# Kernel optimization log

Measured on AMD Instinct MI355X. Metric: run time of the kernel, lower is better.

Reference implementation:

```python
import jax, jax.numpy as jnp
import numpy as np

NEG_INF = -1e9


def setup_inputs() -> dict:
    key = jax.random.key(0)
    ks = jax.random.split(key, 12)
    B, S, D, H = 32, 2048, 512, 512
    enc_outs = jax.random.normal(ks[0], (B, S, D), dtype=jnp.float32)
    num_sent = jnp.maximum(jax.random.randint(ks[1], (B,), 0, S), 1).astype(jnp.int64)
    s = 1.0 / np.sqrt(H)
    return {
        "enc_outs": enc_outs,
        "num_sent": num_sent,
        "num_pred": 8,
        "init_h": jax.random.normal(ks[2], (1, H), dtype=jnp.float32) * s,
        "init_c": jax.random.normal(ks[3], (1, H), dtype=jnp.float32) * s,
        "init_in": jax.random.normal(ks[4], (D,), dtype=jnp.float32) * s,
        "W_ih": jax.random.uniform(ks[5], (4 * H, D), jnp.float32, -s, s),
        "W_hh": jax.random.uniform(ks[6], (4 * H, H), jnp.float32, -s, s),
        "b_ih": jax.random.uniform(ks[7], (4 * H,), jnp.float32, -s, s),
        "b_hh": jax.random.uniform(ks[8], (4 * H,), jnp.float32, -s, s),
        "attn_Wq": jax.random.uniform(ks[9], (H, D), jnp.float32, -s, s),
        "score_W": jax.random.uniform(ks[10], (1, H), jnp.float32, -s, s),
        "score_b": jax.random.uniform(ks[11], (1,), jnp.float32, -s, s),
    }


def reference(enc_outs, num_sent, num_pred, init_h, init_c, init_in,
              W_ih, W_hh, b_ih, b_hh, attn_Wq, score_W, score_b):
    B, S, D = enc_outs.shape
    H = init_h.shape[1]
    # rep_mask: True where sentence index is valid
    mask = jnp.arange(S)[None, :] < num_sent[:, None]  # [B, S]

    def lstm_cell(x, h, c):
        gates = x @ W_ih.T + b_ih + h @ W_hh.T + b_hh  # [B, 4H]
        i, f, g, o = jnp.split(gates, 4, axis=-1)
        i, f, o = jax.nn.sigmoid(i), jax.nn.sigmoid(f), jax.nn.sigmoid(o)
        c_new = f * c + i * jnp.tanh(g)
        return o * jnp.tanh(c_new), c_new

    h0 = jnp.broadcast_to(init_h[0], (B, H))
    c0 = jnp.broadcast_to(init_c[0], (B, H))
    in0 = jnp.broadcast_to(init_in, (B, D))

    def step(carry, _):
        h, c, lstm_in = carry
        h, c = lstm_cell(lstm_in, h, c)
        # glimpse attention: bilinear score, masked softmax over sentences
        q = h @ attn_Wq  # [B, D]
        logits = jnp.einsum('bd,bsd->bs', q, enc_outs)
        logits = jnp.where(mask, logits, NEG_INF)
        attn = jax.nn.softmax(logits, axis=-1)
        out = jnp.einsum('bs,bsd->bd', attn, enc_outs)  # [B, D]
        score = out @ score_W.T + score_b  # [B, 1]
        return (h, c, out), score

    _, scores = jax.lax.scan(step, (h0, c0, in0), None, length=int(num_pred))
    return scores  # [num_pred, B, 1]
```

## Files before the change

kernel.cpp:

```cpp
#include <hip/hip_runtime.h>
#include <math.h>

#define B    32
#define S    2048
#define D    512
#define H    512
#define NP   8
#define NSL  32
#define HSL  16
#define NBT  4
#define BG   8
#define NCH  8
#define SCHUNK 256

__device__ __forceinline__ float sigmoidf_(float x) {
  return 1.0f / (1.0f + __expf(-x));
}

__global__ __launch_bounds__(256)
void k_init(const float* __restrict__ W_ih, const float* __restrict__ W_hh,
            const float* __restrict__ init_h, const float* __restrict__ init_c,
            const float* __restrict__ init_in, const int* __restrict__ ns_raw,
            float* __restrict__ Wt, float* __restrict__ hbuf, float* __restrict__ cbuf,
            float* __restrict__ xin0, int* __restrict__ ns) {
  __shared__ float tbuf[64][65];
  const int blk = blockIdx.x, tid = threadIdx.x;
  const int jt = blk & 31, kt = blk >> 5;
  const int j0 = jt * 64, k0 = kt * 64;
  const int r0 = tid >> 6, cc = tid & 63;
  for (int rr = r0; rr < 64; rr += 4) {
    int j = j0 + rr, k = k0 + cc;
    tbuf[rr][cc] = (k < 512) ? W_ih[(size_t)j * 512 + k]
                             : W_hh[(size_t)j * 512 + (k - 512)];
  }
  __syncthreads();
  for (int rr = r0; rr < 64; rr += 4)
    Wt[(size_t)(k0 + rr) * 2048 + j0 + cc] = tbuf[cc][rr];

  int idx = blk * 256 + tid;
  if (idx < B * H) {
    int d = idx & 511;
    hbuf[idx] = init_h[d];
    cbuf[idx] = init_c[d];
    xin0[idx] = init_in[d];
  }
  if (idx == 0) {
    bool is64 = (ns_raw[1] == 0);
    for (int i = 0; i < B; ++i) ns[i] = is64 ? ns_raw[2 * i] : ns_raw[i];
  }
}

__global__ __launch_bounds__(512, 1)
void k_step(const float* __restrict__ xin0, const float* __restrict__ bih,
            const float* __restrict__ bhh, const float* __restrict__ Wq,
            const float* __restrict__ scW, const float* __restrict__ scb,
            const float* __restrict__ Wt,
            const float* __restrict__ ch_m, const float* __restrict__ ch_l,
            const float* __restrict__ ch_o,
            float* __restrict__ hbuf, float* __restrict__ cbuf,
            float* __restrict__ qpart, float* __restrict__ out, int t) {
  __shared__ float X[BG][1024];
  __shared__ float gacc[8][64][9];
  __shared__ float gl[4][16][8];
  __shared__ float hl[8][16];
  __shared__ float sred[8][8];

  const int tid = threadIdx.x;
  const int sl = blockIdx.x >> 2;
  const int bg = blockIdx.x & 3;
  const int b0 = bg * BG;

  if (t == 0) {
    #pragma unroll
    for (int bl = 0; bl < BG; ++bl)
      X[bl][tid] = xin0[(b0 + bl) * 512 + tid];
  } else {
    const float swd = scW[tid];
    #pragma unroll
    for (int bl = 0; bl < BG; ++bl) {
      const int b = b0 + bl;
      float M = -1e30f;
      #pragma unroll
      for (int c = 0; c < NCH; ++c) M = fmaxf(M, ch_m[b * NCH + c]);
      float e[NCH]; float L = 0.f;
      #pragma unroll
      for (int c = 0; c < NCH; ++c) {
        e[c] = __expf(ch_m[b * NCH + c] - M);
        L += ch_l[b * NCH + c] * e[c];
      }
      float v = 0.f;
      #pragma unroll
      for (int c = 0; c < NCH; ++c)
        v += ch_o[((size_t)(b * NCH + c)) * 512 + tid] * e[c];
      v *= (1.0f / L);
      X[bl][tid] = v;
      float p = v * swd;
      #pragma unroll
      for (int off = 32; off > 0; off >>= 1) p += __shfl_xor(p, off);
      if ((tid & 63) == 0) sred[tid >> 6][bl] = p;
    }
  }
  if (t < NP) {
    const float4* hsrc = (const float4*)(hbuf + (t & 1) * (B * 512));
    #pragma unroll
    for (int it = 0; it < 2; ++it) {
      int idx = it * 512 + tid;
      int bl = idx >> 7;
      int off = idx & 127;
      float4 hv = hsrc[(b0 + bl) * 128 + off];
      *(float4*)&X[bl][512 + off * 4] = hv;
    }
  }
  __syncthreads();

  if (t >= 1 && tid < BG) {
    float s = 0.f;
    #pragma unroll
    for (int w = 0; w < 8; ++w) s += sred[w][tid];
    if (sl == 0) out[(t - 1) * B + b0 + tid] = s + scb[0];
  }
  if (t >= NP) return;

  {
    const int jloc = tid & 63;
    const int kc = tid >> 6;
    const int gi = jloc >> 4, ho = jloc & 15;
    const int jg = gi * 512 + sl * HSL + ho;
    const int k0c = kc * 128;
    const float* wp = Wt + (size_t)k0c * 2048 + jg;
    float acc[BG] = {0, 0, 0, 0, 0, 0, 0, 0};
    for (int kk = 0; kk < 32; ++kk) {
      float wv0 = wp[(size_t)(kk * 4 + 0) * 2048];
      float wv1 = wp[(size_t)(kk * 4 + 1) * 2048];
      float wv2 = wp[(size_t)(kk * 4 + 2) * 2048];
      float wv3 = wp[(size_t)(kk * 4 + 3) * 2048];
      #pragma unroll
      for (int bl = 0; bl < BG; ++bl) {
        const float4 xv = *(const float4*)&X[bl][k0c + kk * 4];
        acc[bl] += wv0 * xv.x + wv1 * xv.y + wv2 * xv.z + wv3 * xv.w;
      }
    }
    #pragma unroll
    for (int bl = 0; bl < BG; ++bl) gacc[kc][jloc][bl] = acc[bl];
  }
  __syncthreads();

  {
    const int bl = tid >> 6, jloc = tid & 63;
    const int gi = jloc >> 4, ho = jloc & 15;
    const int jg = gi * 512 + sl * HSL + ho;
    float g = bih[jg] + bhh[jg];
    #pragma unroll
    for (int kc = 0; kc < 8; ++kc) g += gacc[kc][jloc][bl];
    gl[gi][ho][bl] = g;
  }
  __syncthreads();

  if (tid < 128) {
    const int ho = tid & 15, bl = tid >> 4;
    const int bglob = b0 + bl, hid = sl * HSL + ho;
    float i_ = sigmoidf_(gl[0][ho][bl]);
    float f_ = sigmoidf_(gl[1][ho][bl]);
    float g_ = tanhf(gl[2][ho][bl]);
    float o_ = sigmoidf_(gl[3][ho][bl]);
    float cv = cbuf[bglob * 512 + hid];
    float cn = f_ * cv + i_ * g_;
    cbuf[bglob * 512 + hid] = cn;
    float hv = o_ * tanhf(cn);
    hbuf[((t + 1) & 1) * (B * 512) + bglob * 512 + hid] = hv;
    hl[bl][ho] = hv;
  }
  __syncthreads();

  {
    float w[HSL];
    #pragma unroll
    for (int ho = 0; ho < HSL; ++ho)
      w[ho] = Wq[(size_t)(sl * HSL + ho) * 512 + tid];
    #pragma unroll
    for (int bl = 0; bl < BG; ++bl) {
      float acc = 0.f;
      #pragma unroll
      for (int ho = 0; ho < HSL; ++ho) acc += hl[bl][ho] * w[ho];
      qpart[((size_t)sl * B + b0 + bl) * 512 + tid] = acc;
    }
  }
}

__global__ __launch_bounds__(512, 1)
void k_attn(const float* __restrict__ enc, const float* __restrict__ qpart,
            const int* __restrict__ ns_buf, float* __restrict__ ch_m,
            float* __restrict__ ch_l, float* __restrict__ ch_o) {
  __shared__ float q_lds[512];
  __shared__ float wm[8], wl[8];
  __shared__ float wo[8][512];
  const int b  = blockIdx.x >> 3;
  const int ch = blockIdx.x & 7;
  const int tid = threadIdx.x;
  const int lane = tid & 63;
  const int wv = tid >> 6;

  {
    float s = 0.f;
    #pragma unroll
    for (int sl = 0; sl < NSL; ++sl)
      s += qpart[((size_t)sl * B + b) * 512 + tid];
    q_lds[tid] = s;
  }
  __syncthreads();

  const float4 qa  = *(const float4*)&q_lds[lane * 8];
  const float4 qb4 = *(const float4*)&q_lds[lane * 8 + 4];

  const int s0 = ch * SCHUNK;
  const int nsb = ns_buf[b];
  float m = -1e30f, l = 0.f;
  float o0=0,o1=0,o2=0,o3=0,o4=0,o5=0,o6=0,o7=0;

  const int send = min(s0 + SCHUNK, nsb);
  const size_t rowbase = (size_t)b * S;

  int r = s0 + 2 * wv;
  if (r < send) {
    bool has1 = (r + 1 < send);
    const float4* p0 = (const float4*)(enc + (rowbase + r) * 512 + lane * 8);
    const float4* p1 = (const float4*)(enc + (rowbase + (has1 ? r + 1 : r)) * 512 + lane * 8);
    float4 a0 = p0[0], a1 = p0[1];
    float4 c0 = p1[0], c1 = p1[1];
    while (true) {
      const int rn = r + 16;
      const bool hasn = (rn < send);
      float4 na0, na1, nc0, nc1;
      bool nhas1 = false;
      if (hasn) {
        nhas1 = (rn + 1 < send);
        const float4* f0 = (const float4*)(enc + (rowbase + rn) * 512 + lane * 8);
        const float4* f1 = (const float4*)(enc + (rowbase + (nhas1 ? rn + 1 : rn)) * 512 + lane * 8);
        na0 = f0[0]; na1 = f0[1]; nc0 = f1[0]; nc1 = f1[1];
      }
      float d0 = qa.x*a0.x + qa.y*a0.y + qa.z*a0.z + qa.w*a0.w
               + qb4.x*a1.x + qb4.y*a1.y + qb4.z*a1.z + qb4.w*a1.w;
      float d1 = qa.x*c0.x + qa.y*c0.y + qa.z*c0.z + qa.w*c0.w
               + qb4.x*c1.x + qb4.y*c1.y + qb4.z*c1.z + qb4.w*c1.w;
      #pragma unroll
      for (int off = 32; off > 0; off >>= 1) {
        d0 += __shfl_xor(d0, off);
        d1 += __shfl_xor(d1, off);
      }
      if (!has1) d1 = -1e30f;
      float nm = fmaxf(m, fmaxf(d0, d1));
      float sc = __expf(m - nm);
      float w0 = __expf(d0 - nm);
      float w1 = __expf(d1 - nm);
      l = l * sc + w0 + w1;
      o0 = o0*sc + w0*a0.x + w1*c0.x; o1 = o1*sc + w0*a0.y + w1*c0.y;
      o2 = o2*sc + w0*a0.z + w1*c0.z; o3 = o3*sc + w0*a0.w + w1*c0.w;
      o4 = o4*sc + w0*a1.x + w1*c1.x; o5 = o5*sc + w0*a1.y + w1*c1.y;
      o6 = o6*sc + w0*a1.z + w1*c1.z; o7 = o7*sc + w0*a1.w + w1*c1.w;
      m = nm;
      if (!hasn) break;
      r = rn; has1 = nhas1;
      a0 = na0; a1 = na1; c0 = nc0; c1 = nc1;
    }
  }
  if (lane == 0) { wm[wv] = m; wl[wv] = l; }
  float4* wop = (float4*)&wo[wv][lane * 8];
  wop[0] = make_float4(o0, o1, o2, o3);
  wop[1] = make_float4(o4, o5, o6, o7);
  __syncthreads();

  float M = wm[0];
  #pragma unroll
  for (int w = 1; w < 8; ++w) M = fmaxf(M, wm[w]);
  float e[8]; float L = 0.f;
  #pragma unroll
  for (int w = 0; w < 8; ++w) { e[w] = __expf(wm[w] - M); L += wl[w] * e[w]; }
  if (tid == 0) { ch_m[b * NCH + ch] = M; ch_l[b * NCH + ch] = L; }
  float v = 0.f;
  #pragma unroll
  for (int w = 0; w < 8; ++w) v += wo[w][tid] * e[w];
  ch_o[((size_t)(b * NCH + ch)) * 512 + tid] = v;
}

extern "C" void kernel_launch(void* const* d_in, const int* in_sizes, int n_in,
                              void* d_out, int out_size, void* d_ws, size_t ws_size,
                              hipStream_t stream) {
  const float* enc     = (const float*)d_in[0];
  const int*   ns_raw  = (const int*)d_in[1];
  const float* init_h  = (const float*)d_in[3];
  const float* init_c  = (const float*)d_in[4];
  const float* init_in = (const float*)d_in[5];
  const float* W_ih    = (const float*)d_in[6];
  const float* W_hh    = (const float*)d_in[7];
  const float* b_ih    = (const float*)d_in[8];
  const float* b_hh    = (const float*)d_in[9];
  const float* Wq      = (const float*)d_in[10];
  const float* score_W = (const float*)d_in[11];
  const float* score_b = (const float*)d_in[12];
  float* out = (float*)d_out;

  float* ws    = (float*)d_ws;
  float* Wt    = ws;
  float* hbuf  = ws + 2097152;
  float* cbuf  = ws + 2129920;
  float* xin0  = ws + 2146304;
  float* qpart = ws + 2162688;
  float* ch_m  = ws + 2686976;
  float* ch_l  = ws + 2687232;
  float* ch_o  = ws + 2687488;
  int*   ns    = (int*)(ws + 2818560);

  k_init<<<512, 256, 0, stream>>>(W_ih, W_hh, init_h, init_c, init_in, ns_raw,
                                  Wt, hbuf, cbuf, xin0, ns);
  for (int t = 0; t < NP; ++t) {
    k_step<<<NSL * NBT, 512, 0, stream>>>(xin0, b_ih, b_hh, Wq, score_W, score_b, Wt,
                                          ch_m, ch_l, ch_o, hbuf, cbuf, qpart, out, t);
    k_attn<<<B * NCH, 512, 0, stream>>>(enc, qpart, ns, ch_m, ch_l, ch_o);
  }
  k_step<<<NSL * NBT, 512, 0, stream>>>(xin0, b_ih, b_hh, Wq, score_W, score_b, Wt,
                                        ch_m, ch_l, ch_o, hbuf, cbuf, qpart, out, NP);
}
```

Baseline: 354.1 us.

## Fuse per-step LSTM and attention kernels into one persistent kernel with grid barriers

Replaces the 17 alternating k_step/k_attn launches with a single persistent 256-block kernel that loops over the 8 prediction steps. Stages are separated by a software grid barrier built from agent-scope atomic counters. The cell state and the Wq slice stay in registers across steps, and the batch group per block is halved so 256 blocks cover both phases. This removes per-launch overhead and the final extra step kernel. In exchange it depends on all 256 blocks being co-resident, and it adds atomic polling cost plus relaxed-atomic loads and stores for data passed between blocks.

```diff
diff --git a/kernel.cpp b/kernel.cpp
--- a/kernel.cpp
+++ b/kernel.cpp
@@ -3,26 +3,48 @@
 
 #define B    32
 #define S    2048
-#define D    512
-#define H    512
 #define NP   8
 #define NSL  32
 #define HSL  16
-#define NBT  4
-#define BG   8
+#define BG   4
 #define NCH  8
 #define SCHUNK 256
+#define NBLK 256
+#define NTHR 512
+#define NBAR 16
+
+#define AT_LD(p)   __hip_atomic_load((p), __ATOMIC_RELAXED, __HIP_MEMORY_SCOPE_AGENT)
+#define AT_ST(p,v) __hip_atomic_store((p), (v), __ATOMIC_RELAXED, __HIP_MEMORY_SCOPE_AGENT)
 
 __device__ __forceinline__ float sigmoidf_(float x) {
   return 1.0f / (1.0f + __expf(-x));
 }
 
+__device__ __forceinline__ void gbar(int* cnt, int bi) {
+  asm volatile("s_waitcnt vmcnt(0) lgkmcnt(0)" ::: "memory");
+  __syncthreads();
+  if (threadIdx.x == 0) {
+    int* base = cnt + bi * 128;
+    __hip_atomic_fetch_add(base + (blockIdx.x & 7) * 16, 1,
+                           __ATOMIC_RELAXED, __HIP_MEMORY_SCOPE_AGENT);
+    int s;
+    do {
+      s = 0;
+      #pragma unroll
+      for (int q = 0; q < 8; ++q) s += AT_LD(base + q * 16);
+      if (s < NBLK) __builtin_amdgcn_s_sleep(2);
+    } while (s < NBLK);
+  }
+  __syncthreads();
+  asm volatile("" ::: "memory");
+}
+
 __global__ __launch_bounds__(256)
 void k_init(const float* __restrict__ W_ih, const float* __restrict__ W_hh,
-            const float* __restrict__ init_h, const float* __restrict__ init_c,
-            const float* __restrict__ init_in, const int* __restrict__ ns_raw,
-            float* __restrict__ Wt, float* __restrict__ hbuf, float* __restrict__ cbuf,
-            float* __restrict__ xin0, int* __restrict__ ns) {
+            const float* __restrict__ init_h, const float* __restrict__ init_in,
+            const int* __restrict__ ns_raw,
+            float* __restrict__ Wt, float* __restrict__ hbuf,
+            float* __restrict__ xin0, int* __restrict__ ns, int* __restrict__ cnt) {
   __shared__ float tbuf[64][65];
   const int blk = blockIdx.x, tid = threadIdx.x;
   const int jt = blk & 31, kt = blk >> 5;
@@ -38,248 +60,279 @@
     Wt[(size_t)(k0 + rr) * 2048 + j0 + cc] = tbuf[cc][rr];
 
   int idx = blk * 256 + tid;
-  if (idx < B * H) {
+  if (idx < B * 512) {
     int d = idx & 511;
     hbuf[idx] = init_h[d];
-    cbuf[idx] = init_c[d];
     xin0[idx] = init_in[d];
   }
+  if (idx < NBAR * 128) cnt[idx] = 0;
   if (idx == 0) {
     bool is64 = (ns_raw[1] == 0);
     for (int i = 0; i < B; ++i) ns[i] = is64 ? ns_raw[2 * i] : ns_raw[i];
   }
 }
 
-__global__ __launch_bounds__(512, 1)
-void k_step(const float* __restrict__ xin0, const float* __restrict__ bih,
-            const float* __restrict__ bhh, const float* __restrict__ Wq,
-            const float* __restrict__ scW, const float* __restrict__ scb,
-            const float* __restrict__ Wt,
-            const float* __restrict__ ch_m, const float* __restrict__ ch_l,
-            const float* __restrict__ ch_o,
-            float* __restrict__ hbuf, float* __restrict__ cbuf,
-            float* __restrict__ qpart, float* __restrict__ out, int t) {
+__global__ __launch_bounds__(NTHR, 1)
+void k_persist(const float* __restrict__ enc, const float* __restrict__ init_c,
+               const float* __restrict__ bih, const float* __restrict__ bhh,
+               const float* __restrict__ Wq, const float* __restrict__ scW,
+               const float* __restrict__ scb, const float* __restrict__ Wt,
+               const float* __restrict__ xin0,
+               float* __restrict__ out, float* __restrict__ hbuf,
+               float* __restrict__ qpart, float* __restrict__ ch_m,
+               float* __restrict__ ch_l, float* __restrict__ ch_o,
+               const int* __restrict__ ns, int* __restrict__ cnt) {
   __shared__ float X[BG][1024];
-  __shared__ float gacc[8][64][9];
-  __shared__ float gl[4][16][8];
-  __shared__ float hl[8][16];
-  __shared__ float sred[8][8];
+  __shared__ float gacc[8][64][5];
+  __shared__ float gl[4][HSL][BG];
+  __shared__ float hl[BG][HSL];
+  __shared__ float sred[8][BG];
+  __shared__ float q_lds[512];
+  __shared__ float wm[8], wl[8];
+  __shared__ float wo[8][512];
 
   const int tid = threadIdx.x;
-  const int sl = blockIdx.x >> 2;
-  const int bg = blockIdx.x & 3;
-  const int b0 = bg * BG;
-
-  if (t == 0) {
-    #pragma unroll
-    for (int bl = 0; bl < BG; ++bl)
-      X[bl][tid] = xin0[(b0 + bl) * 512 + tid];
-  } else {
-    const float swd = scW[tid];
-    #pragma unroll
-    for (int bl = 0; bl < BG; ++bl) {
-      const int b = b0 + bl;
-      float M = -1e30f;
-      #pragma unroll
-      for (int c = 0; c < NCH; ++c) M = fmaxf(M, ch_m[b * NCH + c]);
-      float e[NCH]; float L = 0.f;
-      #pragma unroll
-      for (int c = 0; c < NCH; ++c) {
-        e[c] = __expf(ch_m[b * NCH + c] - M);
-        L += ch_l[b * NCH + c] * e[c];
-      }
-      float v = 0.f;
-      #pragma unroll
-      for (int c = 0; c < NCH; ++c)
-        v += ch_o[((size_t)(b * NCH + c)) * 512 + tid] * e[c];
-      v *= (1.0f / L);
-      X[bl][tid] = v;
-      float p = v * swd;
-      #pragma unroll
-      for (int off = 32; off > 0; off >>= 1) p += __shfl_xor(p, off);
-      if ((tid & 63) == 0) sred[tid >> 6][bl] = p;
-    }
-  }
-  if (t < NP) {
-    const float4* hsrc = (const float4*)(hbuf + (t & 1) * (B * 512));
-    #pragma unroll
-    for (int it = 0; it < 2; ++it) {
-      int idx = it * 512 + tid;
-      int bl = idx >> 7;
-      int off = idx & 127;
-      float4 hv = hsrc[(b0 + bl) * 128 + off];
-      *(float4*)&X[bl][512 + off * 4] = hv;
-    }
-  }
-  __syncthreads();
-
-  if (t >= 1 && tid < BG) {
-    float s = 0.f;
-    #pragma unroll
-    for (int w = 0; w < 8; ++w) s += sred[w][tid];
-    if (sl == 0) out[(t - 1) * B + b0 + tid] = s + scb[0];
-  }
-  if (t >= NP) return;
-
-  {
-    const int jloc = tid & 63;
-    const int kc = tid >> 6;
-    const int gi = jloc >> 4, ho = jloc & 15;
-    const int jg = gi * 512 + sl * HSL + ho;
-    const int k0c = kc * 128;
-    const float* wp = Wt + (size_t)k0c * 2048 + jg;
-    float acc[BG] = {0, 0, 0, 0, 0, 0, 0, 0};
-    for (int kk = 0; kk < 32; ++kk) {
-      float wv0 = wp[(size_t)(kk * 4 + 0) * 2048];
-      float wv1 = wp[(size_t)(kk * 4 + 1) * 2048];
-      float wv2 = wp[(size_t)(kk * 4 + 2) * 2048];
-      float wv3 = wp[(size_t)(kk * 4 + 3) * 2048];
+  const int blk = blockIdx.x;
+  const int sl  = blk >> 3;
+  const int bg  = blk & 7;
+  const int b0  = bg * BG;
+  const int ab  = blk >> 3;
+  const int ach = blk & 7;
+  const int lane = tid & 63;
+  const int wv = tid >> 6;
+
+  float wq[HSL];
+  #pragma unroll
+  for (int ho = 0; ho < HSL; ++ho)
+    wq[ho] = Wq[(size_t)(sl * HSL + ho) * 512 + tid];
+  const float swd = scW[tid];
+  const float scb0 = scb[0];
+  float c_reg = (tid < BG * HSL) ? init_c[sl * HSL + (tid & (HSL - 1))] : 0.f;
+  const int nsb = ns[ab];
+  const size_t rowbase = (size_t)ab * S;
+
+  for (int t = 0; t < NP; ++t) {
+    if (t == 0) {
+      #pragma unroll
+      for (int bl = 0; bl < BG; ++bl)
+        X[bl][tid] = xin0[(b0 + bl) * 512 + tid];
+    } else {
       #pragma unroll
       for (int bl = 0; bl < BG; ++bl) {
-        const float4 xv = *(const float4*)&X[bl][k0c + kk * 4];
-        acc[bl] += wv0 * xv.x + wv1 * xv.y + wv2 * xv.z + wv3 * xv.w;
-      }
-    }
-    #pragma unroll
-    for (int bl = 0; bl < BG; ++bl) gacc[kc][jloc][bl] = acc[bl];
-  }
-  __syncthreads();
-
-  {
-    const int bl = tid >> 6, jloc = tid & 63;
-    const int gi = jloc >> 4, ho = jloc & 15;
-    const int jg = gi * 512 + sl * HSL + ho;
-    float g = bih[jg] + bhh[jg];
-    #pragma unroll
-    for (int kc = 0; kc < 8; ++kc) g += gacc[kc][jloc][bl];
-    gl[gi][ho][bl] = g;
-  }
-  __syncthreads();
-
-  if (tid < 128) {
-    const int ho = tid & 15, bl = tid >> 4;
-    const int bglob = b0 + bl, hid = sl * HSL + ho;
-    float i_ = sigmoidf_(gl[0][ho][bl]);
-    float f_ = sigmoidf_(gl[1][ho][bl]);
-    float g_ = tanhf(gl[2][ho][bl]);
-    float o_ = sigmoidf_(gl[3][ho][bl]);
-    float cv = cbuf[bglob * 512 + hid];
-    float cn = f_ * cv + i_ * g_;
-    cbuf[bglob * 512 + hid] = cn;
-    float hv = o_ * tanhf(cn);
-    hbuf[((t + 1) & 1) * (B * 512) + bglob * 512 + hid] = hv;
-    hl[bl][ho] = hv;
-  }
-  __syncthreads();
-
-  {
-    float w[HSL];
-    #pragma unroll
-    for (int ho = 0; ho < HSL; ++ho)
-      w[ho] = Wq[(size_t)(sl * HSL + ho) * 512 + tid];
+        const int b = b0 + bl;
+        float M = -1e30f;
+        #pragma unroll
+        for (int c = 0; c < NCH; ++c) M = fmaxf(M, AT_LD(&ch_m[b * NCH + c]));
+        float e[NCH]; float L = 0.f;
+        #pragma unroll
+        for (int c = 0; c < NCH; ++c) {
+          e[c] = __expf(AT_LD(&ch_m[b * NCH + c]) - M);
+          L += AT_LD(&ch_l[b * NCH + c]) * e[c];
+        }
+        float v = 0.f;
+        #pragma unroll
+        for (int c = 0; c < NCH; ++c)
+          v += AT_LD(&ch_o[((size_t)(b * NCH + c)) * 512 + tid]) * e[c];
+        v *= (1.0f / L);
+        X[bl][tid] = v;
+        float p = v * swd;
+        #pragma unroll
+        for (int off = 32; off > 0; off >>= 1) p += __shfl_xor(p, off);
+        if (lane == 0) sred[wv][bl] = p;
+      }
+    }
+    {
+      const float* hsrc = hbuf + (t & 1) * (B * 512);
+      #pragma unroll
+      for (int i = 0; i < 4; ++i) {
+        int idx = i * 512 + tid;
+        int bl = idx >> 9, off = idx & 511;
+        X[bl][512 + off] = AT_LD(&hsrc[(b0 + bl) * 512 + off]);
+      }
+    }
+    __syncthreads();
+    if (t >= 1 && sl == 0 && tid < BG) {
+      float s = 0.f;
+      #pragma unroll
+      for (int w = 0; w < 8; ++w) s += sred[w][tid];
+      out[(t - 1) * B + b0 + tid] = s + scb0;
+    }
+
+    {
+      const int jloc = tid & 63, kc = tid >> 6;
+      const int gi = jloc >> 4, ho = jloc & 15;
+      const int jg = gi * 512 + sl * HSL + ho;
+      const float* wp = Wt + (size_t)(kc * 128) * 2048 + jg;
+      const int xk0 = kc * 128;
+      float a0 = 0, a1 = 0, a2 = 0, a3 = 0;
+      #pragma unroll 4
+      for (int kk = 0; kk < 32; ++kk) {
+        float w0 = wp[(size_t)(kk * 4 + 0) * 2048];
+        float w1 = wp[(size_t)(kk * 4 + 1) * 2048];
+        float w2 = wp[(size_t)(kk * 4 + 2) * 2048];
+        float w3 = wp[(size_t)(kk * 4 + 3) * 2048];
+        float4 x0 = *(const float4*)&X[0][xk0 + kk * 4];
+        float4 x1 = *(const float4*)&X[1][xk0 + kk * 4];
+        float4 x2 = *(const float4*)&X[2][xk0 + kk * 4];
+        float4 x3 = *(const float4*)&X[3][xk0 + kk * 4];
+        a0 += w0 * x0.x + w1 * x0.y + w2 * x0.z + w3 * x0.w;
+        a1 += w0 * x1.x + w1 * x1.y + w2 * x1.z + w3 * x1.w;
+        a2 += w0 * x2.x + w1 * x2.y + w2 * x2.z + w3 * x2.w;
+        a3 += w0 * x3.x + w1 * x3.y + w2 * x3.z + w3 * x3.w;
+      }
+      gacc[kc][jloc][0] = a0; gacc[kc][jloc][1] = a1;
+      gacc[kc][jloc][2] = a2; gacc[kc][jloc][3] = a3;
+    }
+    __syncthreads();
+
+    if (tid < 256) {
+      const int jloc = tid & 63, bl = tid >> 6;
+      const int gi = jloc >> 4, ho = jloc & 15;
+      const int jg = gi * 512 + sl * HSL + ho;
+      float g = bih[jg] + bhh[jg];
+      #pragma unroll
+      for (int kc = 0; kc < 8; ++kc) g += gacc[kc][jloc][bl];
+      gl[gi][ho][bl] = g;
+    }
+    __syncthreads();
+    if (tid < BG * HSL) {
+      const int bl = tid >> 4, ho = tid & 15;
+      float i_ = sigmoidf_(gl[0][ho][bl]);
+      float f_ = sigmoidf_(gl[1][ho][bl]);
+      float g_ = tanhf(gl[2][ho][bl]);
+      float o_ = sigmoidf_(gl[3][ho][bl]);
+      float cn = f_ * c_reg + i_ * g_;
+      c_reg = cn;
+      float hv = o_ * tanhf(cn);
+      hl[bl][ho] = hv;
+      AT_ST(&hbuf[((t + 1) & 1) * (B * 512) + (b0 + bl) * 512 + sl * HSL + ho], hv);
+    }
+    __syncthreads();
     #pragma unroll
     for (int bl = 0; bl < BG; ++bl) {
       float acc = 0.f;
       #pragma unroll
-      for (int ho = 0; ho < HSL; ++ho) acc += hl[bl][ho] * w[ho];
-      qpart[((size_t)sl * B + b0 + bl) * 512 + tid] = acc;
-    }
-  }
-}
-
-__global__ __launch_bounds__(512, 1)
-void k_attn(const float* __restrict__ enc, const float* __restrict__ qpart,
-            const int* __restrict__ ns_buf, float* __restrict__ ch_m,
-            float* __restrict__ ch_l, float* __restrict__ ch_o) {
-  __shared__ float q_lds[512];
-  __shared__ float wm[8], wl[8];
-  __shared__ float wo[8][512];
-  const int b  = blockIdx.x >> 3;
-  const int ch = blockIdx.x & 7;
-  const int tid = threadIdx.x;
-  const int lane = tid & 63;
-  const int wv = tid >> 6;
-
-  {
-    float s = 0.f;
+      for (int ho = 0; ho < HSL; ++ho) acc += hl[bl][ho] * wq[ho];
+      AT_ST(&qpart[((size_t)sl * B + b0 + bl) * 512 + tid], acc);
+    }
+    gbar(cnt, t * 2 + 0);
+
+    {
+      float s = 0.f;
+      #pragma unroll 8
+      for (int s2 = 0; s2 < NSL; ++s2)
+        s += AT_LD(&qpart[((size_t)s2 * B + ab) * 512 + tid]);
+      q_lds[tid] = s;
+    }
+    __syncthreads();
+
+    {
+      const float4 qa  = *(const float4*)&q_lds[lane * 8];
+      const float4 qb4 = *(const float4*)&q_lds[lane * 8 + 4];
+      const int s0 = ach * SCHUNK;
+      float m = -1e30f, l = 0.f;
+      float o0=0,o1=0,o2=0,o3=0,o4=0,o5=0,o6=0,o7=0;
+      const int send = min(s0 + SCHUNK, nsb);
+
+      int r = s0 + 2 * wv;
+      if (r < send) {
+        bool has1 = (r + 1 < send);
+        const float4* p0 = (const float4*)(enc + (rowbase + r) * 512 + lane * 8);
+        const float4* p1 = (const float4*)(enc + (rowbase + (has1 ? r + 1 : r)) * 512 + lane * 8);
+        float4 a0 = p0[0], a1 = p0[1];
+        float4 c0 = p1[0], c1 = p1[1];
+        while (true) {
+          const int rn = r + 16;
+          const bool hasn = (rn < send);
+          float4 na0, na1, nc0, nc1;
+          bool nhas1 = false;
+          if (hasn) {
+            nhas1 = (rn + 1 < send);
+            const float4* f0 = (const float4*)(enc + (rowbase + rn) * 512 + lane * 8);
+            const float4* f1 = (const float4*)(enc + (rowbase + (nhas1 ? rn + 1 : rn)) * 512 + lane * 8);
+            na0 = f0[0]; na1 = f0[1]; nc0 = f1[0]; nc1 = f1[1];
+          }
+          float d0 = qa.x*a0.x + qa.y*a0.y + qa.z*a0.z + qa.w*a0.w
+                   + qb4.x*a1.x + qb4.y*a1.y + qb4.z*a1.z + qb4.w*a1.w;
+          float d1 = qa.x*c0.x + qa.y*c0.y + qa.z*c0.z + qa.w*c0.w
+                   + qb4.x*c1.x + qb4.y*c1.y + qb4.z*c1.z + qb4.w*c1.w;
+          #pragma unroll
+          for (int off = 32; off > 0; off >>= 1) {
+            d0 += __shfl_xor(d0, off);
+            d1 += __shfl_xor(d1, off);
+          }
+          if (!has1) d1 = -1e30f;
+          float nm = fmaxf(m, fmaxf(d0, d1));
+          float sc = __expf(m - nm);
+          float w0 = __expf(d0 - nm);
+          float w1 = __expf(d1 - nm);
+          l = l * sc + w0 + w1;
+          o0 = o0*sc + w0*a0.x + w1*c0.x; o1 = o1*sc + w0*a0.y + w1*c0.y;
+          o2 = o2*sc + w0*a0.z + w1*c0.z; o3 = o3*sc + w0*a0.w + w1*c0.w;
+          o4 = o4*sc + w0*a1.x + w1*c1.x; o5 = o5*sc + w0*a1.y + w1*c1.y;
+          o6 = o6*sc + w0*a1.z + w1*c1.z; o7 = o7*sc + w0*a1.w + w1*c1.w;
+          m = nm;
+          if (!hasn) break;
+          r = rn; has1 = nhas1;
+          a0 = na0; a1 = na1; c0 = nc0; c1 = nc1;
+        }
+      }
+      if (lane == 0) { wm[wv] = m; wl[wv] = l; }
+      float4* wop = (float4*)&wo[wv][lane * 8];
+      wop[0] = make_float4(o0, o1, o2, o3);
+      wop[1] = make_float4(o4, o5, o6, o7);
+      __syncthreads();
+
+      float M = wm[0];
+      #pragma unroll
+      for (int w = 1; w < 8; ++w) M = fmaxf(M, wm[w]);
+      float e[8]; float L = 0.f;
+      #pragma unroll
+      for (int w = 0; w < 8; ++w) { e[w] = __expf(wm[w] - M); L += wl[w] * e[w]; }
+      if (tid == 0) {
+        AT_ST(&ch_m[ab * NCH + ach], M);
+        AT_ST(&ch_l[ab * NCH + ach], L);
+      }
+      float v = 0.f;
+      #pragma unroll
+      for (int w = 0; w < 8; ++w) v += wo[w][tid] * e[w];
+      AT_ST(&ch_o[((size_t)(ab * NCH + ach)) * 512 + tid], v);
+    }
+    gbar(cnt, t * 2 + 1);
+  }
+
+  if (blk < 8) {
+    const int fb0 = blk * BG;
     #pragma unroll
-    for (int sl = 0; sl < NSL; ++sl)
-      s += qpart[((size_t)sl * B + b) * 512 + tid];
-    q_lds[tid] = s;
-  }
-  __syncthreads();
-
-  const float4 qa  = *(const float4*)&q_lds[lane * 8];
-  const float4 qb4 = *(const float4*)&q_lds[lane * 8 + 4];
-
-  const int s0 = ch * SCHUNK;
-  const int nsb = ns_buf[b];
-  float m = -1e30f, l = 0.f;
-  float o0=0,o1=0,o2=0,o3=0,o4=0,o5=0,o6=0,o7=0;
-
-  const int send = min(s0 + SCHUNK, nsb);
-  const size_t rowbase = (size_t)b * S;
-
-  int r = s0 + 2 * wv;
-  if (r < send) {
-    bool has1 = (r + 1 < send);
-    const float4* p0 = (const float4*)(enc + (rowbase + r) * 512 + lane * 8);
-    const float4* p1 = (const float4*)(enc + (rowbase + (has1 ? r + 1 : r)) * 512 + lane * 8);
-    float4 a0 = p0[0], a1 = p0[1];
-    float4 c0 = p1[0], c1 = p1[1];
-    while (true) {
-      const int rn = r + 16;
-      const bool hasn = (rn < send);
-      float4 na0, na1, nc0, nc1;
-      bool nhas1 = false;
-      if (hasn) {
-        nhas1 = (rn + 1 < send);
-        const float4* f0 = (const float4*)(enc + (rowbase + rn) * 512 + lane * 8);
-        const float4* f1 = (const float4*)(enc + (rowbase + (nhas1 ? rn + 1 : rn)) * 512 + lane * 8);
-        na0 = f0[0]; na1 = f0[1]; nc0 = f1[0]; nc1 = f1[1];
-      }
-      float d0 = qa.x*a0.x + qa.y*a0.y + qa.z*a0.z + qa.w*a0.w
-               + qb4.x*a1.x + qb4.y*a1.y + qb4.z*a1.z + qb4.w*a1.w;
-      float d1 = qa.x*c0.x + qa.y*c0.y + qa.z*c0.z + qa.w*c0.w
-               + qb4.x*c1.x + qb4.y*c1.y + qb4.z*c1.z + qb4.w*c1.w;
-      #pragma unroll
-      for (int off = 32; off > 0; off >>= 1) {
-        d0 += __shfl_xor(d0, off);
-        d1 += __shfl_xor(d1, off);
-      }
-      if (!has1) d1 = -1e30f;
-      float nm = fmaxf(m, fmaxf(d0, d1));
-      float sc = __expf(m - nm);
-      float w0 = __expf(d0 - nm);
-      float w1 = __expf(d1 - nm);
-      l = l * sc + w0 + w1;
-      o0 = o0*sc + w0*a0.x + w1*c0.x; o1 = o1*sc + w0*a0.y + w1*c0.y;
-      o2 = o2*sc + w0*a0.z + w1*c0.z; o3 = o3*sc + w0*a0.w + w1*c0.w;
-      o4 = o4*sc + w0*a1.x + w1*c1.x; o5 = o5*sc + w0*a1.y + w1*c1.y;
-      o6 = o6*sc + w0*a1.z + w1*c1.z; o7 = o7*sc + w0*a1.w + w1*c1.w;
-      m = nm;
-      if (!hasn) break;
-      r = rn; has1 = nhas1;
-      a0 = na0; a1 = na1; c0 = nc0; c1 = nc1;
-    }
-  }
-  if (lane == 0) { wm[wv] = m; wl[wv] = l; }
-  float4* wop = (float4*)&wo[wv][lane * 8];
-  wop[0] = make_float4(o0, o1, o2, o3);
-  wop[1] = make_float4(o4, o5, o6, o7);
-  __syncthreads();
-
-  float M = wm[0];
-  #pragma unroll
-  for (int w = 1; w < 8; ++w) M = fmaxf(M, wm[w]);
-  float e[8]; float L = 0.f;
-  #pragma unroll
-  for (int w = 0; w < 8; ++w) { e[w] = __expf(wm[w] - M); L += wl[w] * e[w]; }
-  if (tid == 0) { ch_m[b * NCH + ch] = M; ch_l[b * NCH + ch] = L; }
-  float v = 0.f;
-  #pragma unroll
-  for (int w = 0; w < 8; ++w) v += wo[w][tid] * e[w];
-  ch_o[((size_t)(b * NCH + ch)) * 512 + tid] = v;
+    for (int bl = 0; bl < BG; ++bl) {
+      const int b = fb0 + bl;
+      float M = -1e30f;
+      #pragma unroll
+      for (int c = 0; c < NCH; ++c) M = fmaxf(M, AT_LD(&ch_m[b * NCH + c]));
+      float e[NCH]; float L = 0.f;
+      #pragma unroll
+      for (int c = 0; c < NCH; ++c) {
+        e[c] = __expf(AT_LD(&ch_m[b * NCH + c]) - M);
+        L += AT_LD(&ch_l[b * NCH + c]) * e[c];
+      }
+      float v = 0.f;
+      #pragma unroll
+      for (int c = 0; c < NCH; ++c)
+        v += AT_LD(&ch_o[((size_t)(b * NCH + c)) * 512 + tid]) * e[c];
+      v *= (1.0f / L);
+      float p = v * swd;
+      #pragma unroll
+      for (int off = 32; off > 0; off >>= 1) p += __shfl_xor(p, off);
+      if (lane == 0) sred[wv][bl] = p;
+    }
+    __syncthreads();
+    if (tid < BG) {
+      float s = 0.f;
+      #pragma unroll
+      for (int w = 0; w < 8; ++w) s += sred[w][tid];
+      out[(NP - 1) * B + fb0 + tid] = s + scb0;
+    }
+  }
 }
 
 extern "C" void kernel_launch(void* const* d_in, const int* in_sizes, int n_in,
@@ -302,21 +355,17 @@
   float* ws    = (float*)d_ws;
   float* Wt    = ws;
   float* hbuf  = ws + 2097152;
-  float* cbuf  = ws + 2129920;
-  float* xin0  = ws + 2146304;
-  float* qpart = ws + 2162688;
-  float* ch_m  = ws + 2686976;
-  float* ch_l  = ws + 2687232;
-  float* ch_o  = ws + 2687488;
-  int*   ns    = (int*)(ws + 2818560);
-
-  k_init<<<512, 256, 0, stream>>>(W_ih, W_hh, init_h, init_c, init_in, ns_raw,
-                                  Wt, hbuf, cbuf, xin0, ns);
-  for (int t = 0; t < NP; ++t) {
-    k_step<<<NSL * NBT, 512, 0, stream>>>(xin0, b_ih, b_hh, Wq, score_W, score_b, Wt,
-                                          ch_m, ch_l, ch_o, hbuf, cbuf, qpart, out, t);
-    k_attn<<<B * NCH, 512, 0, stream>>>(enc, qpart, ns, ch_m, ch_l, ch_o);
-  }
-  k_step<<<NSL * NBT, 512, 0, stream>>>(xin0, b_ih, b_hh, Wq, score_W, score_b, Wt,
-                                        ch_m, ch_l, ch_o, hbuf, cbuf, qpart, out, NP);
-}
+  float* xin0  = ws + 2129920;
+  float* qpart = ws + 2146304;
+  float* ch_m  = ws + 2670592;
+  float* ch_l  = ws + 2670848;
+  float* ch_o  = ws + 2671104;
+  int*   ns    = (int*)(ws + 2802176);
+  int*   cnt   = (int*)(ws + 2802208);
+
+  k_init<<<512, 256, 0, stream>>>(W_ih, W_hh, init_h, init_in, ns_raw,
+                                  Wt, hbuf, xin0, ns, cnt);
+  k_persist<<<NBLK, NTHR, 0, stream>>>(enc, init_c, b_ih, b_hh, Wq, score_W, score_b,
+                                       Wt, xin0, out, hbuf, qpart,
+                                       ch_m, ch_l, ch_o, ns, cnt);
+}
```

Result: slower. 402.4 us (+13.6%).

## Split step kernel into reduce and gate kernels with gate-interleaved float4 weights

Applied to the files above, without the earlier changes.

Splits the per-step kernel into a separate attention-output reduction kernel and a gates kernel. Weights are re-laid out so the four LSTM gates of one hidden unit sit in one float4, and biases are pre-summed. The gates kernel now uses 256 blocks of 8 hidden units and reads x and h straight from global memory instead of staging them in LDS. This aims to raise parallelism and weight-load width, at the cost of an extra launch per step and a qpart reduction over 64 partials instead of 32 in the attention kernel.

```diff
diff --git a/kernel.cpp b/kernel.cpp
--- a/kernel.cpp
+++ b/kernel.cpp
@@ -3,46 +3,52 @@
 
 #define B    32
 #define S    2048
-#define D    512
-#define H    512
 #define NP   8
-#define NSL  32
-#define HSL  16
-#define NBT  4
-#define BG   8
 #define NCH  8
 #define SCHUNK 256
+#define HG   64
+#define BGP  4
 
 __device__ __forceinline__ float sigmoidf_(float x) {
   return 1.0f / (1.0f + __expf(-x));
 }
 
 __global__ __launch_bounds__(256)
-void k_init(const float* __restrict__ W_ih, const float* __restrict__ W_hh,
-            const float* __restrict__ init_h, const float* __restrict__ init_c,
-            const float* __restrict__ init_in, const int* __restrict__ ns_raw,
-            float* __restrict__ Wt, float* __restrict__ hbuf, float* __restrict__ cbuf,
-            float* __restrict__ xin0, int* __restrict__ ns) {
-  __shared__ float tbuf[64][65];
+void k_initW(const float* __restrict__ W_ih, const float* __restrict__ W_hh,
+             float4* __restrict__ Wt4) {
+  __shared__ float tb[4][64][65];
   const int blk = blockIdx.x, tid = threadIdx.x;
-  const int jt = blk & 31, kt = blk >> 5;
-  const int j0 = jt * 64, k0 = kt * 64;
+  const int ht = blk & 7, kt = blk >> 3;
+  const int h0 = ht * 64, k0 = kt * 64;
   const int r0 = tid >> 6, cc = tid & 63;
-  for (int rr = r0; rr < 64; rr += 4) {
-    int j = j0 + rr, k = k0 + cc;
-    tbuf[rr][cc] = (k < 512) ? W_ih[(size_t)j * 512 + k]
-                             : W_hh[(size_t)j * 512 + (k - 512)];
-  }
-  __syncthreads();
-  for (int rr = r0; rr < 64; rr += 4)
-    Wt[(size_t)(k0 + rr) * 2048 + j0 + cc] = tbuf[cc][rr];
-
-  int idx = blk * 256 + tid;
-  if (idx < B * H) {
-    int d = idx & 511;
-    hbuf[idx] = init_h[d];
-    cbuf[idx] = init_c[d];
-    xin0[idx] = init_in[d];
+  const float* W = (k0 < 512) ? W_ih : W_hh;
+  const int kk0 = (k0 < 512) ? k0 : (k0 - 512);
+  #pragma unroll
+  for (int gi = 0; gi < 4; ++gi)
+    for (int rr = r0; rr < 64; rr += 4)
+      tb[gi][rr][cc] = W[(size_t)(gi * 512 + h0 + rr) * 512 + kk0 + cc];
+  __syncthreads();
+  for (int kk = r0; kk < 64; kk += 4)
+    Wt4[(size_t)(k0 + kk) * 512 + h0 + cc] =
+        make_float4(tb[0][cc][kk], tb[1][cc][kk], tb[2][cc][kk], tb[3][cc][kk]);
+}
+
+__global__ __launch_bounds__(256)
+void k_init2(const float* __restrict__ init_h, const float* __restrict__ init_c,
+             const float* __restrict__ init_in, const float* __restrict__ b_ih,
+             const float* __restrict__ b_hh, const int* __restrict__ ns_raw,
+             float* __restrict__ hbuf, float* __restrict__ cbuf,
+             float* __restrict__ xin, float4* __restrict__ bias4, int* __restrict__ ns) {
+  const int idx = blockIdx.x * 256 + threadIdx.x;
+  const int d = idx & 511;
+  hbuf[idx] = init_h[d];
+  cbuf[idx] = init_c[d];
+  xin[idx]  = init_in[d];
+  if (idx < 512) {
+    bias4[idx] = make_float4(b_ih[idx]        + b_hh[idx],
+                             b_ih[512 + idx]  + b_hh[512 + idx],
+                             b_ih[1024 + idx] + b_hh[1024 + idx],
+                             b_ih[1536 + idx] + b_hh[1536 + idx]);
   }
   if (idx == 0) {
     bool is64 = (ns_raw[1] == 0);
@@ -50,144 +56,108 @@
   }
 }
 
-__global__ __launch_bounds__(512, 1)
-void k_step(const float* __restrict__ xin0, const float* __restrict__ bih,
-            const float* __restrict__ bhh, const float* __restrict__ Wq,
-            const float* __restrict__ scW, const float* __restrict__ scb,
-            const float* __restrict__ Wt,
-            const float* __restrict__ ch_m, const float* __restrict__ ch_l,
-            const float* __restrict__ ch_o,
-            float* __restrict__ hbuf, float* __restrict__ cbuf,
-            float* __restrict__ qpart, float* __restrict__ out, int t) {
-  __shared__ float X[BG][1024];
-  __shared__ float gacc[8][64][9];
-  __shared__ float gl[4][16][8];
-  __shared__ float hl[8][16];
-  __shared__ float sred[8][8];
-
+__global__ __launch_bounds__(512)
+void k_reduceX(const float* __restrict__ ch_m, const float* __restrict__ ch_l,
+               const float* __restrict__ ch_o, const float* __restrict__ scW,
+               const float* __restrict__ scb, float* __restrict__ xin,
+               float* __restrict__ out, int t) {
+  __shared__ float red[512];
+  const int b = blockIdx.x, tid = threadIdx.x;
+  float M = -1e30f;
+  #pragma unroll
+  for (int c = 0; c < NCH; ++c) M = fmaxf(M, ch_m[b * NCH + c]);
+  float e[NCH]; float L = 0.f;
+  #pragma unroll
+  for (int c = 0; c < NCH; ++c) {
+    e[c] = __expf(ch_m[b * NCH + c] - M);
+    L += ch_l[b * NCH + c] * e[c];
+  }
+  float v = 0.f;
+  #pragma unroll
+  for (int c = 0; c < NCH; ++c)
+    v += ch_o[((size_t)(b * NCH + c)) * 512 + tid] * e[c];
+  v *= (1.0f / L);
+  if (t < NP) xin[b * 512 + tid] = v;
+  red[tid] = v * scW[tid];
+  __syncthreads();
+  for (int st = 256; st > 0; st >>= 1) {
+    if (tid < st) red[tid] += red[tid + st];
+    __syncthreads();
+  }
+  if (tid == 0) out[(t - 1) * B + b] = red[0] + scb[0];
+}
+
+__global__ __launch_bounds__(512)
+void k_gates(const float4* __restrict__ Wt4, const float4* __restrict__ bias4,
+             const float* __restrict__ xin, const float* __restrict__ Wq,
+             float* __restrict__ hbuf, float* __restrict__ cbuf,
+             float* __restrict__ qpart, int t) {
+  __shared__ float4 gacc[8][64];
+  __shared__ float hl[8][8];
   const int tid = threadIdx.x;
-  const int sl = blockIdx.x >> 2;
-  const int bg = blockIdx.x & 3;
-  const int b0 = bg * BG;
-
-  if (t == 0) {
+  const int hg = blockIdx.x >> 2, bgp = blockIdx.x & 3;
+  const int b0 = bgp * 8;
+  const int lane = tid & 63, kc = tid >> 6;
+  const int ho = lane & 7, bl = lane >> 3;
+  const int hid = hg * 8 + ho;
+  const float* hprev = hbuf + (t & 1) * (B * 512);
+  const float* Xsrc = (kc < 4) ? xin : hprev;
+  const int xoff = (b0 + bl) * 512 + (kc & 3) * 128;
+  const float4* wp = Wt4 + (size_t)(kc * 128) * 512 + hid;
+
+  float4 acc = make_float4(0.f, 0.f, 0.f, 0.f);
+  #pragma unroll 4
+  for (int kk = 0; kk < 128; kk += 4) {
+    const float4 xv = *(const float4*)&Xsrc[xoff + kk];
+    const float4 w0 = wp[(size_t)(kk + 0) * 512];
+    const float4 w1 = wp[(size_t)(kk + 1) * 512];
+    const float4 w2 = wp[(size_t)(kk + 2) * 512];
+    const float4 w3 = wp[(size_t)(kk + 3) * 512];
+    acc.x += w0.x * xv.x + w1.x * xv.y + w2.x * xv.z + w3.x * xv.w;
+    acc.y += w0.y * xv.x + w1.y * xv.y + w2.y * xv.z + w3.y * xv.w;
+    acc.z += w0.z * xv.x + w1.z * xv.y + w2.z * xv.z + w3.z * xv.w;
+    acc.w += w0.w * xv.x + w1.w * xv.y + w2.w * xv.z + w3.w * xv.w;
+  }
+  gacc[kc][lane] = acc;
+  __syncthreads();
+
+  if (tid < 64) {
+    const int ho2 = tid & 7, bl2 = tid >> 3;
+    const int hid2 = hg * 8 + ho2;
+    float4 s = gacc[0][tid];
     #pragma unroll
-    for (int bl = 0; bl < BG; ++bl)
-      X[bl][tid] = xin0[(b0 + bl) * 512 + tid];
-  } else {
-    const float swd = scW[tid];
+    for (int k2 = 1; k2 < 8; ++k2) {
+      float4 g = gacc[k2][tid];
+      s.x += g.x; s.y += g.y; s.z += g.z; s.w += g.w;
+    }
+    const float4 bb = bias4[hid2];
+    float i_ = sigmoidf_(s.x + bb.x);
+    float f_ = sigmoidf_(s.y + bb.y);
+    float g_ = tanhf(s.z + bb.z);
+    float o_ = sigmoidf_(s.w + bb.w);
+    const int cidx = (b0 + bl2) * 512 + hid2;
+    float cn = f_ * cbuf[cidx] + i_ * g_;
+    cbuf[cidx] = cn;
+    float hv = o_ * tanhf(cn);
+    hbuf[((t + 1) & 1) * (B * 512) + cidx] = hv;
+    hl[bl2][ho2] = hv;
+  }
+  __syncthreads();
+
+  float wqv[8];
+  #pragma unroll
+  for (int h2 = 0; h2 < 8; ++h2)
+    wqv[h2] = Wq[(size_t)(hg * 8 + h2) * 512 + tid];
+  #pragma unroll
+  for (int bl2 = 0; bl2 < 8; ++bl2) {
+    float a = 0.f;
     #pragma unroll
-    for (int bl = 0; bl < BG; ++bl) {
-      const int b = b0 + bl;
-      float M = -1e30f;
-      #pragma unroll
-      for (int c = 0; c < NCH; ++c) M = fmaxf(M, ch_m[b * NCH + c]);
-      float e[NCH]; float L = 0.f;
-      #pragma unroll
-      for (int c = 0; c < NCH; ++c) {
-        e[c] = __expf(ch_m[b * NCH + c] - M);
-        L += ch_l[b * NCH + c] * e[c];
-      }
-      float v = 0.f;
-      #pragma unroll
-      for (int c = 0; c < NCH; ++c)
-        v += ch_o[((size_t)(b * NCH + c)) * 512 + tid] * e[c];
-      v *= (1.0f / L);
-      X[bl][tid] = v;
-      float p = v * swd;
-      #pragma unroll
-      for (int off = 32; off > 0; off >>= 1) p += __shfl_xor(p, off);
-      if ((tid & 63) == 0) sred[tid >> 6][bl] = p;
-    }
-  }
-  if (t < NP) {
-    const float4* hsrc = (const float4*)(hbuf + (t & 1) * (B * 512));
-    #pragma unroll
-    for (int it = 0; it < 2; ++it) {
-      int idx = it * 512 + tid;
-      int bl = idx >> 7;
-      int off = idx & 127;
-      float4 hv = hsrc[(b0 + bl) * 128 + off];
-      *(float4*)&X[bl][512 + off * 4] = hv;
-    }
-  }
-  __syncthreads();
-
-  if (t >= 1 && tid < BG) {
-    float s = 0.f;
-    #pragma unroll
-    for (int w = 0; w < 8; ++w) s += sred[w][tid];
-    if (sl == 0) out[(t - 1) * B + b0 + tid] = s + scb[0];
-  }
-  if (t >= NP) return;
-
-  {
-    const int jloc = tid & 63;
-    const int kc = tid >> 6;
-    const int gi = jloc >> 4, ho = jloc & 15;
-    const int jg = gi * 512 + sl * HSL + ho;
-    const int k0c = kc * 128;
-    const float* wp = Wt + (size_t)k0c * 2048 + jg;
-    float acc[BG] = {0, 0, 0, 0, 0, 0, 0, 0};
-    for (int kk = 0; kk < 32; ++kk) {
-      float wv0 = wp[(size_t)(kk * 4 + 0) * 2048];
-      float wv1 = wp[(size_t)(kk * 4 + 1) * 2048];
-      float wv2 = wp[(size_t)(kk * 4 + 2) * 2048];
-      float wv3 = wp[(size_t)(kk * 4 + 3) * 2048];
-      #pragma unroll
-      for (int bl = 0; bl < BG; ++bl) {
-        const float4 xv = *(const float4*)&X[bl][k0c + kk * 4];
-        acc[bl] += wv0 * xv.x + wv1 * xv.y + wv2 * xv.z + wv3 * xv.w;
-      }
-    }
-    #pragma unroll
-    for (int bl = 0; bl < BG; ++bl) gacc[kc][jloc][bl] = acc[bl];
-  }
-  __syncthreads();
-
-  {
-    const int bl = tid >> 6, jloc = tid & 63;
-    const int gi = jloc >> 4, ho = jloc & 15;
-    const int jg = gi * 512 + sl * HSL + ho;
-    float g = bih[jg] + bhh[jg];
-    #pragma unroll
-    for (int kc = 0; kc < 8; ++kc) g += gacc[kc][jloc][bl];
-    gl[gi][ho][bl] = g;
-  }
-  __syncthreads();
-
-  if (tid < 128) {
-    const int ho = tid & 15, bl = tid >> 4;
-    const int bglob = b0 + bl, hid = sl * HSL + ho;
-    float i_ = sigmoidf_(gl[0][ho][bl]);
-    float f_ = sigmoidf_(gl[1][ho][bl]);
-    float g_ = tanhf(gl[2][ho][bl]);
-    float o_ = sigmoidf_(gl[3][ho][bl]);
-    float cv = cbuf[bglob * 512 + hid];
-    float cn = f_ * cv + i_ * g_;
-    cbuf[bglob * 512 + hid] = cn;
-    float hv = o_ * tanhf(cn);
-    hbuf[((t + 1) & 1) * (B * 512) + bglob * 512 + hid] = hv;
-    hl[bl][ho] = hv;
-  }
-  __syncthreads();
-
-  {
-    float w[HSL];
-    #pragma unroll
-    for (int ho = 0; ho < HSL; ++ho)
-      w[ho] = Wq[(size_t)(sl * HSL + ho) * 512 + tid];
-    #pragma unroll
-    for (int bl = 0; bl < BG; ++bl) {
-      float acc = 0.f;
-      #pragma unroll
-      for (int ho = 0; ho < HSL; ++ho) acc += hl[bl][ho] * w[ho];
-      qpart[((size_t)sl * B + b0 + bl) * 512 + tid] = acc;
-    }
-  }
-}
-
-__global__ __launch_bounds__(512, 1)
+    for (int h2 = 0; h2 < 8; ++h2) a += hl[bl2][h2] * wqv[h2];
+    qpart[((size_t)hg * B + b0 + bl2) * 512 + tid] = a;
+  }
+}
+
+__global__ __launch_bounds__(512)
 void k_attn(const float* __restrict__ enc, const float* __restrict__ qpart,
             const int* __restrict__ ns_buf, float* __restrict__ ch_m,
             float* __restrict__ ch_l, float* __restrict__ ch_o) {
@@ -202,9 +172,9 @@
 
   {
     float s = 0.f;
-    #pragma unroll
-    for (int sl = 0; sl < NSL; ++sl)
-      s += qpart[((size_t)sl * B + b) * 512 + tid];
+    #pragma unroll 8
+    for (int hg = 0; hg < HG; ++hg)
+      s += qpart[((size_t)hg * B + b) * 512 + tid];
     q_lds[tid] = s;
   }
   __syncthreads();
@@ -299,24 +269,26 @@
   const float* score_b = (const float*)d_in[12];
   float* out = (float*)d_out;
 
-  float* ws    = (float*)d_ws;
-  float* Wt    = ws;
-  float* hbuf  = ws + 2097152;
-  float* cbuf  = ws + 2129920;
-  float* xin0  = ws + 2146304;
-  float* qpart = ws + 2162688;
-  float* ch_m  = ws + 2686976;
-  float* ch_l  = ws + 2687232;
-  float* ch_o  = ws + 2687488;
-  int*   ns    = (int*)(ws + 2818560);
-
-  k_init<<<512, 256, 0, stream>>>(W_ih, W_hh, init_h, init_c, init_in, ns_raw,
-                                  Wt, hbuf, cbuf, xin0, ns);
+  float* ws     = (float*)d_ws;
+  float4* Wt4   = (float4*)ws;
+  float4* bias4 = (float4*)(ws + 2097152);
+  float*  hbuf  = ws + 2099200;
+  float*  cbuf  = ws + 2131968;
+  float*  xin   = ws + 2148352;
+  float*  qpart = ws + 2164736;
+  float*  ch_m  = ws + 3213312;
+  float*  ch_l  = ws + 3213568;
+  float*  ch_o  = ws + 3213824;
+  int*    ns    = (int*)(ws + 3344896);
+
+  k_initW<<<128, 256, 0, stream>>>(W_ih, W_hh, Wt4);
+  k_init2<<<64, 256, 0, stream>>>(init_h, init_c, init_in, b_ih, b_hh, ns_raw,
+                                  hbuf, cbuf, xin, bias4, ns);
   for (int t = 0; t < NP; ++t) {
-    k_step<<<NSL * NBT, 512, 0, stream>>>(xin0, b_ih, b_hh, Wq, score_W, score_b, Wt,
-                                          ch_m, ch_l, ch_o, hbuf, cbuf, qpart, out, t);
+    if (t > 0)
+      k_reduceX<<<B, 512, 0, stream>>>(ch_m, ch_l, ch_o, score_W, score_b, xin, out, t);
+    k_gates<<<HG * BGP, 512, 0, stream>>>(Wt4, bias4, xin, Wq, hbuf, cbuf, qpart, t);
     k_attn<<<B * NCH, 512, 0, stream>>>(enc, qpart, ns, ch_m, ch_l, ch_o);
   }
-  k_step<<<NSL * NBT, 512, 0, stream>>>(xin0, b_ih, b_hh, Wq, score_W, score_b, Wt,
-                                        ch_m, ch_l, ch_o, hbuf, cbuf, qpart, out, NP);
-}
+  k_reduceX<<<B, 512, 0, stream>>>(ch_m, ch_l, ch_o, score_W, score_b, xin, out, NP);
+}
```

Result: slower. 461.3 us (+30.3%).

## Split attention into more sequence chunks and deepen enc prefetch to two pairs

Applied to the files above, without the earlier changes.

The attention kernel now splits each batch row's sequence into 16 chunks of 128 instead of 8 of 256, doubling the grid so more blocks can fill the GPU. Launch bounds allow two blocks per CU. The streaming loop is restructured into a counted loop that keeps two row-pairs of prefetched loads in flight instead of one, to hide more memory latency. The trade-off is higher register pressure, more partial results for the step kernel to merge, and a reworked workspace layout.

```diff
diff --git a/kernel.cpp b/kernel.cpp
--- a/kernel.cpp
+++ b/kernel.cpp
@@ -10,8 +10,8 @@
 #define HSL  16
 #define NBT  4
 #define BG   8
-#define NCH  8
-#define SCHUNK 256
+#define NCH  16
+#define SCHUNK 128
 
 __device__ __forceinline__ float sigmoidf_(float x) {
   return 1.0f / (1.0f + __expf(-x));
@@ -187,22 +187,22 @@
   }
 }
 
-__global__ __launch_bounds__(512, 1)
+__global__ __launch_bounds__(512, 2)
 void k_attn(const float* __restrict__ enc, const float* __restrict__ qpart,
             const int* __restrict__ ns_buf, float* __restrict__ ch_m,
             float* __restrict__ ch_l, float* __restrict__ ch_o) {
   __shared__ float q_lds[512];
   __shared__ float wm[8], wl[8];
   __shared__ float wo[8][512];
-  const int b  = blockIdx.x >> 3;
-  const int ch = blockIdx.x & 7;
+  const int b  = blockIdx.x >> 4;
+  const int ch = blockIdx.x & 15;
   const int tid = threadIdx.x;
   const int lane = tid & 63;
   const int wv = tid >> 6;
 
   {
     float s = 0.f;
-    #pragma unroll
+    #pragma unroll 8
     for (int sl = 0; sl < NSL; ++sl)
       s += qpart[((size_t)sl * B + b) * 512 + tid];
     q_lds[tid] = s;
@@ -214,55 +214,60 @@
 
   const int s0 = ch * SCHUNK;
   const int nsb = ns_buf[b];
+  const int send = min(s0 + SCHUNK, nsb);
+  const size_t rowbase = (size_t)b * S;
+  const int first = s0 + 2 * wv;
+  const int npair = (first < send) ? ((send - first + 15) >> 4) : 0;
+
   float m = -1e30f, l = 0.f;
   float o0=0,o1=0,o2=0,o3=0,o4=0,o5=0,o6=0,o7=0;
 
-  const int send = min(s0 + SCHUNK, nsb);
-  const size_t rowbase = (size_t)b * S;
-
-  int r = s0 + 2 * wv;
-  if (r < send) {
-    bool has1 = (r + 1 < send);
-    const float4* p0 = (const float4*)(enc + (rowbase + r) * 512 + lane * 8);
-    const float4* p1 = (const float4*)(enc + (rowbase + (has1 ? r + 1 : r)) * 512 + lane * 8);
-    float4 a0 = p0[0], a1 = p0[1];
-    float4 c0 = p1[0], c1 = p1[1];
-    while (true) {
-      const int rn = r + 16;
-      const bool hasn = (rn < send);
-      float4 na0, na1, nc0, nc1;
-      bool nhas1 = false;
-      if (hasn) {
-        nhas1 = (rn + 1 < send);
-        const float4* f0 = (const float4*)(enc + (rowbase + rn) * 512 + lane * 8);
-        const float4* f1 = (const float4*)(enc + (rowbase + (nhas1 ? rn + 1 : rn)) * 512 + lane * 8);
-        na0 = f0[0]; na1 = f0[1]; nc0 = f1[0]; nc1 = f1[1];
-      }
-      float d0 = qa.x*a0.x + qa.y*a0.y + qa.z*a0.z + qa.w*a0.w
-               + qb4.x*a1.x + qb4.y*a1.y + qb4.z*a1.z + qb4.w*a1.w;
-      float d1 = qa.x*c0.x + qa.y*c0.y + qa.z*c0.z + qa.w*c0.w
-               + qb4.x*c1.x + qb4.y*c1.y + qb4.z*c1.z + qb4.w*c1.w;
-      #pragma unroll
-      for (int off = 32; off > 0; off >>= 1) {
-        d0 += __shfl_xor(d0, off);
-        d1 += __shfl_xor(d1, off);
-      }
-      if (!has1) d1 = -1e30f;
-      float nm = fmaxf(m, fmaxf(d0, d1));
-      float sc = __expf(m - nm);
-      float w0 = __expf(d0 - nm);
-      float w1 = __expf(d1 - nm);
-      l = l * sc + w0 + w1;
-      o0 = o0*sc + w0*a0.x + w1*c0.x; o1 = o1*sc + w0*a0.y + w1*c0.y;
-      o2 = o2*sc + w0*a0.z + w1*c0.z; o3 = o3*sc + w0*a0.w + w1*c0.w;
-      o4 = o4*sc + w0*a1.x + w1*c1.x; o5 = o5*sc + w0*a1.y + w1*c1.y;
-      o6 = o6*sc + w0*a1.z + w1*c1.z; o7 = o7*sc + w0*a1.w + w1*c1.w;
-      m = nm;
-      if (!hasn) break;
-      r = rn; has1 = nhas1;
-      a0 = na0; a1 = na1; c0 = nc0; c1 = nc1;
-    }
-  }
+  float4 A0, A1, A2, A3, B0, B1, B2, B3;
+  bool av = false, bv = false;
+
+#define LOADP(i, x0, x1, x2, x3, v)                                          \
+  {                                                                          \
+    const int r_ = first + 16 * (i);                                         \
+    (v) = (r_ + 1 < send);                                                   \
+    const float4* p0_ = (const float4*)(enc + (rowbase + r_) * 512 + lane * 8); \
+    const float4* p1_ = (const float4*)(enc + (rowbase + ((v) ? r_ + 1 : r_)) * 512 + lane * 8); \
+    (x0) = p0_[0]; (x1) = p0_[1]; (x2) = p1_[0]; (x3) = p1_[1];              \
+  }
+
+  if (npair > 0) LOADP(0, A0, A1, A2, A3, av);
+  if (npair > 1) LOADP(1, B0, B1, B2, B3, bv);
+
+  for (int i = 0; i < npair; ++i) {
+    float4 C0 = A0, C1 = A1, C2 = A2, C3 = A3;
+    bool cv = false;
+    if (i + 2 < npair) LOADP(i + 2, C0, C1, C2, C3, cv);
+
+    float d0 = qa.x*A0.x + qa.y*A0.y + qa.z*A0.z + qa.w*A0.w
+             + qb4.x*A1.x + qb4.y*A1.y + qb4.z*A1.z + qb4.w*A1.w;
+    float d1 = qa.x*A2.x + qa.y*A2.y + qa.z*A2.z + qa.w*A2.w
+             + qb4.x*A3.x + qb4.y*A3.y + qb4.z*A3.z + qb4.w*A3.w;
+    #pragma unroll
+    for (int off = 32; off > 0; off >>= 1) {
+      d0 += __shfl_xor(d0, off);
+      d1 += __shfl_xor(d1, off);
+    }
+    if (!av) d1 = -1e30f;
+    float nm = fmaxf(m, fmaxf(d0, d1));
+    float sc = __expf(m - nm);
+    float w0 = __expf(d0 - nm);
+    float w1 = __expf(d1 - nm);
+    l = l * sc + w0 + w1;
+    o0 = o0*sc + w0*A0.x + w1*A2.x; o1 = o1*sc + w0*A0.y + w1*A2.y;
+    o2 = o2*sc + w0*A0.z + w1*A2.z; o3 = o3*sc + w0*A0.w + w1*A2.w;
+    o4 = o4*sc + w0*A1.x + w1*A3.x; o5 = o5*sc + w0*A1.y + w1*A3.y;
+    o6 = o6*sc + w0*A1.z + w1*A3.z; o7 = o7*sc + w0*A1.w + w1*A3.w;
+    m = nm;
+
+    A0 = B0; A1 = B1; A2 = B2; A3 = B3; av = bv;
+    B0 = C0; B1 = C1; B2 = C2; B3 = C3; bv = cv;
+  }
+#undef LOADP
+
   if (lane == 0) { wm[wv] = m; wl[wv] = l; }
   float4* wop = (float4*)&wo[wv][lane * 8];
   wop[0] = make_float4(o0, o1, o2, o3);
@@ -306,9 +311,9 @@
   float* xin0  = ws + 2146304;
   float* qpart = ws + 2162688;
   float* ch_m  = ws + 2686976;
-  float* ch_l  = ws + 2687232;
-  float* ch_o  = ws + 2687488;
-  int*   ns    = (int*)(ws + 2818560);
+  float* ch_l  = ws + 2687488;
+  float* ch_o  = ws + 2688000;
+  int*   ns    = (int*)(ws + 2950144);
 
   k_init<<<512, 256, 0, stream>>>(W_ih, W_hh, init_h, init_c, init_in, ns_raw,
                                   Wt, hbuf, cbuf, xin0, ns);
```

After: 365.8 us. 3.3% more time.
